# Kernel tuning notes

Hardware: AMD Instinct MI355X
Metric: run time of the kernel (lower is better)

The kernel has to match this reference:

```python
import jax, jax.numpy as jnp
import numpy as np

NEG_INF = -1e30  # log-domain 'zero' (avoid -inf for numerical safety)


def ctc_loss(labels, logits, label_length, logit_length, blank_index=0):
    """Per-example CTC negative log-likelihood.

    labels:       [B, L] int, dense, padded (values != blank within label_length)
    logits:       [T, B, V] float, time-major (TF ctc_loss_v2 default)
    label_length: [B] int
    logit_length: [B] int
    returns:      [B] float, -log p(labels | logits)
    """
    T, B, V = logits.shape
    L = labels.shape[1]
    S = 2 * L + 1  # extended label sequence: blank, l1, blank, l2, ..., blank

    logp = jax.nn.log_softmax(logits, axis=-1)  # [T, B, V]

    # Extended label sequence per batch element: ext[:, 0::2] = blank, ext[:, 1::2] = labels
    ext = jnp.full((B, S), blank_index, dtype=labels.dtype)
    ext = ext.at[:, 1::2].set(labels)  # [B, S]

    # Emission log-probs for each extended position: emit[t, b, s] = logp[t, b, ext[b, s]]
    emit = jnp.take_along_axis(
        logp, jnp.broadcast_to(ext[None].astype(jnp.int32), (T, B, S)), axis=2
    )  # [T, B, S]

    # Skip transition s-2 -> s allowed iff ext[s] != blank and ext[s] != ext[s-2]
    ext_m2 = jnp.concatenate(
        [jnp.full((B, 2), -1, dtype=labels.dtype), ext[:, :-2]], axis=1
    )
    skip_ok = (ext != blank_index) & (ext != ext_m2)  # [B, S]

    def shift(a, k):
        # shift right along S by k, filling with NEG_INF
        return jnp.concatenate(
            [jnp.full((B, k), NEG_INF, dtype=a.dtype), a[:, :-k]], axis=1
        )

    # alpha at t=0: only positions 0 (blank) and 1 (first label) are reachable
    alpha0 = jnp.full((B, S), NEG_INF, dtype=logits.dtype)
    alpha0 = alpha0.at[:, 0].set(emit[0, :, 0]).at[:, 1].set(emit[0, :, 1])

    def step(alpha, xs):
        emit_t, t = xs  # emit_t: [B, S], t: scalar time index
        cand = jnp.stack(
            [alpha, shift(alpha, 1), jnp.where(skip_ok, shift(alpha, 2), NEG_INF)],
            axis=0,
        )  # [3, B, S]
        new = jax.nn.logsumexp(cand, axis=0) + emit_t
        # Freeze alpha for samples whose logit sequence has ended
        new = jnp.where((t < logit_length)[:, None], new, alpha)
        return new, None

    ts = jnp.arange(1, T)
    alpha, _ = jax.lax.scan(step, alpha0, (emit[1:], ts))  # [B, S]

    b = jnp.arange(B)
    end = 2 * label_length  # index of trailing blank for each sample
    ll = jnp.logaddexp(alpha[b, end], alpha[b, jnp.maximum(end - 1, 0)])
    return -ll  # [B]


def setup_inputs() -> dict:
    key = jax.random.key(0)
    k1, k2, k3 = jax.random.split(key, 3)
    T, B, V, L = 1024, 64, 256, 256
    logits = jax.random.normal(k1, (T, B, V), dtype=jnp.float32)
    # labels avoid the blank index (0)
    labels = jax.random.randint(k2, (B, L), 1, V, dtype=jnp.int32)
    label_length = jax.random.randint(k3, (B,), L // 2, L + 1, dtype=jnp.int32)
    logit_length = jnp.full((B,), T, dtype=jnp.int32)
    return {
        "labels": labels,
        "logits": logits,
        "label_length": label_length,
        "logit_length": logit_length,
    }


def reference(labels, logits, label_length, logit_length):
    # CTCLossEndpointCpu: loss = reduce_mean(ctc_loss_v2(...)) with blank_index=0
    per_example = ctc_loss(labels, logits, label_length, logit_length, blank_index=0)
    return jnp.mean(per_example)
```

## Files before the change

### kernel.cpp

```cpp
#include <hip/hip_runtime.h>
#include <math.h>


constexpr int V = 256;
constexpr float LN2_F = 0.6931471805599453f;

typedef unsigned uint2v __attribute__((ext_vector_type(2)));

template <int CTRL>
__device__ __forceinline__ float dpp_mov_f(float x) {
    return __int_as_float(__builtin_amdgcn_update_dpp(
        0, __float_as_int(x), CTRL, 0xF, 0xF, true));
}

__device__ __forceinline__ float wave_shr1_f(float x) {
    return __int_as_float(__builtin_amdgcn_update_dpp(
        0, __float_as_int(x), 0x138, 0xF, 0xF, true));
}

__device__ __forceinline__ float wave_max_f(float m) {
    m = fmaxf(m, dpp_mov_f<0xB1>(m));
    m = fmaxf(m, dpp_mov_f<0x4E>(m));
    m = fmaxf(m, dpp_mov_f<0x124>(m));
    m = fmaxf(m, dpp_mov_f<0x128>(m));
#if __has_builtin(__builtin_amdgcn_permlane16_swap) && __has_builtin(__builtin_amdgcn_permlane32_swap)
    uint2v a = __builtin_amdgcn_permlane16_swap(__float_as_uint(m),
                                                __float_as_uint(m), false, false);
    m = fmaxf(__uint_as_float(a.x), __uint_as_float(a.y));
    uint2v b = __builtin_amdgcn_permlane32_swap(__float_as_uint(m),
                                                __float_as_uint(m), false, false);
    m = fmaxf(__uint_as_float(b.x), __uint_as_float(b.y));
#else
    m = fmaxf(m, __shfl_xor(m, 16, 64));
    m = fmaxf(m, __shfl_xor(m, 32, 64));
#endif
    return m;
}

__device__ __forceinline__ float wave_sum_f(float s) {
    s += dpp_mov_f<0xB1>(s);
    s += dpp_mov_f<0x4E>(s);
    s += dpp_mov_f<0x124>(s);
    s += dpp_mov_f<0x128>(s);
#if __has_builtin(__builtin_amdgcn_permlane16_swap) && __has_builtin(__builtin_amdgcn_permlane32_swap)
    uint2v a = __builtin_amdgcn_permlane16_swap(__float_as_uint(s),
                                                __float_as_uint(s), false, false);
    s = __uint_as_float(a.x) + __uint_as_float(a.y);
    uint2v b = __builtin_amdgcn_permlane32_swap(__float_as_uint(s),
                                                __float_as_uint(s), false, false);
    s = __uint_as_float(b.x) + __uint_as_float(b.y);
#else
    s += __shfl_xor(s, 16, 64);
    s += __shfl_xor(s, 32, 64);
#endif
    return s;
}

#define MACS(EB, E1, E3, E5, E7) do {                                  \
    const float c7m = wave_shr1_f(cur7);                               \
    curT = (curT + cur7) * (EB);                                       \
    cur7 = fmaf(sk7, cur5, cur7 + cur6) * (E7);                        \
    cur6 = (cur6 + cur5) * (EB);                                       \
    cur5 = fmaf(sk5, cur3, cur5 + cur4) * (E5);                        \
    cur4 = (cur4 + cur3) * (EB);                                       \
    cur3 = fmaf(sk3, cur1, cur3 + cur2) * (E3);                        \
    cur2 = (cur2 + cur1) * (EB);                                       \
    cur1 = fmaf(sk1, c7m, cur1 + cur0) * (E1);                         \
    cur0 = (cur0 + c7m) * (EB);                                        \
  } while (0)

#define RENORM do {                                                    \
    curT *= mkT; cur0 *= mk0; cur1 *= mk1; cur2 *= mk2; cur3 *= mk3;   \
    cur4 *= mk4; cur5 *= mk5; cur6 *= mk6; cur7 *= mk7;                \
    float _m = fmaxf(curT, cur0); _m = fmaxf(_m, cur1);                \
    _m = fmaxf(_m, cur2); _m = fmaxf(_m, cur3); _m = fmaxf(_m, cur4);  \
    _m = fmaxf(_m, cur5); _m = fmaxf(_m, cur6); _m = fmaxf(_m, cur7);  \
    _m = wave_max_f(_m);                                               \
    const float _inv = 1.f / fmaxf(_m, 1e-30f);                        \
    log2acc -= log2f(_inv);                                            \
    curT *= _inv; cur0 *= _inv; cur1 *= _inv; cur2 *= _inv;            \
    cur3 *= _inv; cur4 *= _inv; cur5 *= _inv; cur6 *= _inv;            \
    cur7 *= _inv;                                                      \
  } while (0)

#define DECLSET(N) float g##N##a = 0, g##N##b = 0, g##N##c = 0,        \
                         g##N##d = 0, g##N##e = 0
#define PRE(N, S) do {                                                 \
    const float* _er = er + 256 * (S);                                 \
    g##N##a = _er[ix]; g##N##b = _er[iy];                              \
    g##N##c = _er[iz]; g##N##d = _er[iw];                              \
    g##N##e = _er[0];                                                  \
  } while (0)
#define STEPR(N, S) do {                                               \
    MACS(g##N##e, g##N##a, g##N##b, g##N##c, g##N##d);                 \
    PRE(N, S);                                                         \
  } while (0)
#define STEPC(N) MACS(g##N##e, g##N##a, g##N##b, g##N##c, g##N##d)

#define WG_BARRIER asm volatile("s_waitcnt lgkmcnt(0)\n\ts_barrier" ::: "memory")

__global__ __launch_bounds__(1024) void ctc_main(
    const int*   __restrict__ labels,
    const float* __restrict__ logits,
    const int*   __restrict__ label_len,
    const int*   __restrict__ logit_len,
    float*       __restrict__ vres,
    int T, int B, int L)
{
    const int tid = threadIdx.x;
    const int wid = tid >> 6;
    const int l   = tid & 63;
    const int b   = blockIdx.x;

    __shared__ __align__(16) float erow[2][16][256];
    __shared__ float afin[514];
    __shared__ float accbuf[16];

    const int Tb = logit_len[b];
    const int Lb = label_len[b];
    const int NW = Tb / 16;

    const float* lg = logits + (size_t)b * V;
    const size_t rs = (size_t)B * V;

    if (wid == 0) {
        __builtin_amdgcn_s_setprio(1);
        const int Sb = 2 * Lb + 1;

        const int4 lb4 = ((const int4*)(labels + (size_t)b * L))[l];
        const int ix = lb4.x, iy = lb4.y, iz = lb4.z, iw = lb4.w;
        const int prevw = __shfl_up(iw, 1);
        const float sk1 = (l > 0 && ix != prevw) ? 1.f : 0.f;
        const float sk3 = (iy != ix) ? 1.f : 0.f;
        const float sk5 = (iz != iy) ? 1.f : 0.f;
        const float sk7 = (iw != iz) ? 1.f : 0.f;

        const float mk0 = (8 * l + 0 < Sb) ? 1.f : 0.f;
        const float mk1 = (8 * l + 1 < Sb) ? 1.f : 0.f;
        const float mk2 = (8 * l + 2 < Sb) ? 1.f : 0.f;
        const float mk3 = (8 * l + 3 < Sb) ? 1.f : 0.f;
        const float mk4 = (8 * l + 4 < Sb) ? 1.f : 0.f;
        const float mk5 = (8 * l + 5 < Sb) ? 1.f : 0.f;
        const float mk6 = (8 * l + 6 < Sb) ? 1.f : 0.f;
        const float mk7 = (8 * l + 7 < Sb) ? 1.f : 0.f;
        const float mkT = (Sb > 512 && l == 63) ? 1.f : 0.f;

        float cur0 = 0.f, cur1 = 0.f, cur2 = 0.f, cur3 = 0.f;
        float cur4 = 0.f, cur5 = 0.f, cur6 = 0.f, cur7 = 0.f, curT = 0.f;
        if (l == 0) {
            cur0 = __expf(lg[0]);
            cur1 = __expf(lg[ix]) * mk1;
        }
        float log2acc = 0.f;

        DECLSET(0); DECLSET(1); DECLSET(2); DECLSET(3);
        DECLSET(4); DECLSET(5); DECLSET(6); DECLSET(7);

        for (int k = 0; k <= NW; ++k) {
            if (k >= 1) {
                const int w = k - 1;
                const float* er = &erow[w & 1][0][0];
                if (w == 0) {
                    PRE(1, 1); PRE(2, 2); PRE(3, 3); PRE(4, 4);
                    PRE(5, 5); PRE(6, 6); PRE(7, 7); PRE(0, 8);
                    STEPR(1, 9);  STEPR(2, 10); STEPR(3, 11); STEPR(4, 12);
                    STEPR(5, 13); STEPR(6, 14); STEPR(7, 15);
                    STEPC(0);
                    STEPC(1); STEPC(2); STEPC(3); STEPC(4);
                    STEPC(5); STEPC(6); STEPC(7);
                } else {
                    PRE(0, 0); PRE(1, 1); PRE(2, 2); PRE(3, 3);
                    PRE(4, 4); PRE(5, 5); PRE(6, 6); PRE(7, 7);
                    STEPR(0, 8);  STEPR(1, 9);  STEPR(2, 10); STEPR(3, 11);
                    STEPR(4, 12); STEPR(5, 13); STEPR(6, 14); STEPR(7, 15);
                    STEPC(0); STEPC(1); STEPC(2); STEPC(3);
                    STEPC(4); STEPC(5); STEPC(6); STEPC(7);
                }
                RENORM;
            }
            WG_BARRIER;
        }

        for (int t = 16 * NW; t < Tb; ++t) {
            if (t < 1) continue;
            const float* rowp = lg + rs * (size_t)t;
            const float eb = __expf(rowp[0]);
            const float e1 = __expf(rowp[ix]), e3 = __expf(rowp[iy]);
            const float e5 = __expf(rowp[iz]), e7 = __expf(rowp[iw]);
            MACS(eb, e1, e3, e5, e7);
        }

        afin[8 * l + 0] = cur0; afin[8 * l + 1] = cur1;
        afin[8 * l + 2] = cur2; afin[8 * l + 3] = cur3;
        afin[8 * l + 4] = cur4; afin[8 * l + 5] = cur5;
        afin[8 * l + 6] = cur6; afin[8 * l + 7] = cur7;
        if (l == 63) afin[512] = curT;
        const int end = 2 * Lb;
        const int em1 = (end > 0) ? end - 1 : 0;
        float ssum = afin[end] + afin[em1];
        ssum = fmaxf(ssum, 1e-37f);
        const float lnt = logf(ssum) + LN2_F * log2acc;

        WG_BARRIER;

        float c = 0.f;
        #pragma unroll
        for (int q = 0; q < 16; ++q) c += accbuf[q];
        if (l == 0) vres[b] = c - lnt;
    } else {
        const int s0   = wid - 1;
        const bool dual = (wid == 15);
        float accA = 0.f, accB = 0.f;

        float4 pc0{}, pn0{}, pc1{}, pn1{};
        if (NW > 0) {
            pc0 = *(const float4*)(lg + rs * (size_t)s0 + 4 * l);
            pn0 = *(const float4*)(lg + rs * (size_t)(16 + s0) + 4 * l);
            if (dual) {
                pc1 = *(const float4*)(lg + rs * (size_t)15 + 4 * l);
                pn1 = *(const float4*)(lg + rs * (size_t)31 + 4 * l);
            }
        }

        for (int k = 0; k <= NW; ++k) {
            if (k < NW) {
                const int hh = k & 1;
                const float4 x0 = pc0;
                pc0 = pn0;
                if (k + 2 < NW)
                    pn0 = *(const float4*)(lg + rs * (size_t)(16 * (k + 2) + s0) + 4 * l);
                float4 x1{};
                if (dual) {
                    x1 = pc1;
                    pc1 = pn1;
                    if (k + 2 < NW)
                        pn1 = *(const float4*)(lg + rs * (size_t)(16 * (k + 2) + 15) + 4 * l);
                }
                float4 e0;
                e0.x = __expf(x0.x); e0.y = __expf(x0.y);
                e0.z = __expf(x0.z); e0.w = __expf(x0.w);
                *(float4*)&erow[hh][s0][4 * l] = e0;
                if (dual) {
                    float4 e1v;
                    e1v.x = __expf(x1.x); e1v.y = __expf(x1.y);
                    e1v.z = __expf(x1.z); e1v.w = __expf(x1.w);
                    *(float4*)&erow[hh][15][4 * l] = e1v;
                }
                {
                    float m = fmaxf(fmaxf(x0.x, x0.y), fmaxf(x0.z, x0.w));
                    m = wave_max_f(m);
                    float ss = __expf(x0.x - m) + __expf(x0.y - m) +
                               __expf(x0.z - m) + __expf(x0.w - m);
                    ss = wave_sum_f(ss);
                    const int t = 16 * k + s0;
                    if (t < Tb) accA += m + logf(ss);
                }
                if (dual) {
                    float m = fmaxf(fmaxf(x1.x, x1.y), fmaxf(x1.z, x1.w));
                    m = wave_max_f(m);
                    float ss = __expf(x1.x - m) + __expf(x1.y - m) +
                               __expf(x1.z - m) + __expf(x1.w - m);
                    ss = wave_sum_f(ss);
                    const int t = 16 * k + 15;
                    if (t < Tb) accB += m + logf(ss);
                }
            }
            WG_BARRIER;
        }

        for (int t = 16 * NW + s0; t < Tb; t += 16) {
            const float4 x = *(const float4*)(lg + rs * (size_t)t + 4 * l);
            float m = fmaxf(fmaxf(x.x, x.y), fmaxf(x.z, x.w));
            m = wave_max_f(m);
            float ss = __expf(x.x - m) + __expf(x.y - m) +
                       __expf(x.z - m) + __expf(x.w - m);
            ss = wave_sum_f(ss);
            accA += m + logf(ss);
        }
        if (dual) {
            for (int t = 16 * NW + 15; t < Tb; t += 16) {
                const float4 x = *(const float4*)(lg + rs * (size_t)t + 4 * l);
                float m = fmaxf(fmaxf(x.x, x.y), fmaxf(x.z, x.w));
                m = wave_max_f(m);
                float ss = __expf(x.x - m) + __expf(x.y - m) +
                           __expf(x.z - m) + __expf(x.w - m);
                ss = wave_sum_f(ss);
                accB += m + logf(ss);
            }
        }
        if (l == 0) {
            accbuf[s0] = accA;
            if (dual) accbuf[15] = accB;
        }
        WG_BARRIER;
    }
}

__global__ __launch_bounds__(64) void ctc_final(
    const float* __restrict__ vres,
    float* __restrict__ out, int B)
{
    const int b = threadIdx.x;
    float v = (b < B) ? vres[b] : 0.f;
    #pragma unroll
    for (int o = 32; o >= 1; o >>= 1) v += __shfl_xor(v, o, 64);
    if (threadIdx.x == 0) out[0] = v / (float)B;
}

#define FB_PRE(N, S) do {                                              \
    G##N = *(const float4*)(&gbuf[h][S][l][0]);                        \
    A##N = bbuf[h][S];                                                 \
  } while (0)
#define FB_STEPR(N, S) do {                                            \
    MACS(A##N, G##N.x, G##N.y, G##N.z, G##N.w);                        \
    FB_PRE(N, S);                                                      \
  } while (0)
#define FB_STEPC(N) MACS(A##N, G##N.x, G##N.y, G##N.z, G##N.w)

#define FB_PLOAD(dst, WV, J)                                           \
    dst = *(const float4*)(lg + rs * (size_t)(16 * (WV) + p + 7 * (J)) + 4 * l)
#define FB_PROC(XV, i) do {                                            \
    float4 _e;                                                         \
    _e.x = __expf((XV).x); _e.y = __expf((XV).y);                      \
    _e.z = __expf((XV).z); _e.w = __expf((XV).w);                      \
    *(float4*)&prow[p][4 * l] = _e;                                    \
    const float* _pr = prow[p];                                        \
    float _gb = _pr[0];                                                \
    float4 _gv;                                                        \
    _gv.x = _pr[ix]; _gv.y = _pr[iy]; _gv.z = _pr[iz]; _gv.w = _pr[iw];\
    *(float4*)&gbuf[h][i][l][0] = _gv;                                 \
    if (l == 0) bbuf[h][i] = _gb;                                      \
  } while (0)

__global__ __launch_bounds__(512) void fb_ctc_main(
    const int*   __restrict__ labels,
    const float* __restrict__ logits,
    const int*   __restrict__ label_len,
    const int*   __restrict__ logit_len,
    float*       __restrict__ partial,
    float*       __restrict__ lnterm,
    int T, int B, int L)
{
    const int tid = threadIdx.x;
    const int wid = tid >> 6;
    const int l   = tid & 63;

    if ((int)blockIdx.x < B) {
        __shared__ __align__(16) float gbuf[2][16][64][4];
        __shared__ float bbuf[2][16];
        __shared__ __align__(16) float prow[7][256];
        __shared__ float afin[514];

        const int b = blockIdx.x;
        const int Tb = logit_len[b];
        const int Lb = label_len[b];
        const int Sb = 2 * Lb + 1;

        const float* lg = logits + (size_t)b * V;
        const size_t rs = (size_t)B * V;

        const int4 lb4 = ((const int4*)(labels + (size_t)b * L))[l];
        const int ix = lb4.x, iy = lb4.y, iz = lb4.z, iw = lb4.w;
        const int prevw = __shfl_up(iw, 1);
        const float sk1 = (l > 0 && ix != prevw) ? 1.f : 0.f;
        const float sk3 = (iy != ix) ? 1.f : 0.f;
        const float sk5 = (iz != iy) ? 1.f : 0.f;
        const float sk7 = (iw != iz) ? 1.f : 0.f;

        const float mk0 = (8 * l + 0 < Sb) ? 1.f : 0.f;
        const float mk1 = (8 * l + 1 < Sb) ? 1.f : 0.f;
        const float mk2 = (8 * l + 2 < Sb) ? 1.f : 0.f;
        const float mk3 = (8 * l + 3 < Sb) ? 1.f : 0.f;
        const float mk4 = (8 * l + 4 < Sb) ? 1.f : 0.f;
        const float mk5 = (8 * l + 5 < Sb) ? 1.f : 0.f;
        const float mk6 = (8 * l + 6 < Sb) ? 1.f : 0.f;
        const float mk7 = (8 * l + 7 < Sb) ? 1.f : 0.f;
        const float mkT = (Sb > 512 && l == 63) ? 1.f : 0.f;

        float cur0 = 0.f, cur1 = 0.f, cur2 = 0.f, cur3 = 0.f;
        float cur4 = 0.f, cur5 = 0.f, cur6 = 0.f, cur7 = 0.f, curT = 0.f;
        if (l == 0) {
            cur0 = __expf(lg[0]);
            cur1 = __expf(lg[ix]) * mk1;
        }
        float log2acc = 0.f;

        const int NW = Tb / 16;

        float4 G0{}, G1{}, G2{}, G3{}, G4{}, G5{}, G6{}, G7{};
        float  A0 = 0, A1 = 0, A2 = 0, A3 = 0, A4 = 0, A5 = 0, A6 = 0, A7 = 0;

        const int p = (wid > 0) ? wid - 1 : 0;
        const bool three = (p < 2);
        float4 ca{}, cb{}, cc{}, na{}, nb{}, nc{};
        if (wid > 0 && NW > 0) {
            FB_PLOAD(ca, 0, 0);
            FB_PLOAD(cb, 0, 1);
            if (three) FB_PLOAD(cc, 0, 2);
        }
        if (wid == 0) __builtin_amdgcn_s_setprio(1);

        for (int k = 0; k <= NW; ++k) {
            if (wid != 0) {
                if (k < NW) {
                    const int h = k & 1;
                    if (k + 1 < NW) {
                        FB_PLOAD(na, k + 1, 0);
                        FB_PLOAD(nb, k + 1, 1);
                        if (three) FB_PLOAD(nc, k + 1, 2);
                    }
                    FB_PROC(ca, p);
                    FB_PROC(cb, p + 7);
                    if (three) FB_PROC(cc, p + 14);
                    ca = na; cb = nb; cc = nc;
                }
            } else if (k >= 1) {
                const int w = k - 1;
                const int h = w & 1;
                if (w == 0) {
                    FB_PRE(1, 1); FB_PRE(2, 2); FB_PRE(3, 3); FB_PRE(4, 4);
                    FB_PRE(5, 5); FB_PRE(6, 6); FB_PRE(7, 7); FB_PRE(0, 8);
                    FB_STEPR(1, 9);  FB_STEPR(2, 10); FB_STEPR(3, 11);
                    FB_STEPR(4, 12); FB_STEPR(5, 13); FB_STEPR(6, 14);
                    FB_STEPR(7, 15);
                    FB_STEPC(0);
                    FB_STEPC(1); FB_STEPC(2); FB_STEPC(3); FB_STEPC(4);
                    FB_STEPC(5); FB_STEPC(6); FB_STEPC(7);
                } else {
                    FB_PRE(0, 0); FB_PRE(1, 1); FB_PRE(2, 2); FB_PRE(3, 3);
                    FB_PRE(4, 4); FB_PRE(5, 5); FB_PRE(6, 6); FB_PRE(7, 7);
                    FB_STEPR(0, 8);  FB_STEPR(1, 9);  FB_STEPR(2, 10);
                    FB_STEPR(3, 11); FB_STEPR(4, 12); FB_STEPR(5, 13);
                    FB_STEPR(6, 14); FB_STEPR(7, 15);
                    FB_STEPC(0); FB_STEPC(1); FB_STEPC(2); FB_STEPC(3);
                    FB_STEPC(4); FB_STEPC(5); FB_STEPC(6); FB_STEPC(7);
                }
                RENORM;
            }
            WG_BARRIER;
        }

        if (wid == 0) {
            for (int t = 16 * NW; t < Tb; ++t) {
                if (t < 1) continue;
                const float* rowp = lg + rs * (size_t)t;
                const float eb = __expf(rowp[0]);
                const float e1 = __expf(rowp[ix]), e3 = __expf(rowp[iy]);
                const float e5 = __expf(rowp[iz]), e7 = __expf(rowp[iw]);
                MACS(eb, e1, e3, e5, e7);
            }

            afin[8 * l + 0] = cur0; afin[8 * l + 1] = cur1;
            afin[8 * l + 2] = cur2; afin[8 * l + 3] = cur3;
            afin[8 * l + 4] = cur4; afin[8 * l + 5] = cur5;
            afin[8 * l + 6] = cur6; afin[8 * l + 7] = cur7;
            if (l == 63) afin[512] = curT;
            const int end = 2 * Lb;
            const int em1 = (end > 0) ? end - 1 : 0;
            float ssum = afin[end] + afin[em1];
            ssum = fmaxf(ssum, 1e-37f);
            if (l == 0) lnterm[b] = logf(ssum) + LN2_F * log2acc;
        }
    } else {
        const int w  = ((int)blockIdx.x - B) * 8 + wid;
        const int nW = ((int)gridDim.x - B) * 8;
        const int rows = T * B;
        const int bb = w % B;
        const int Tbb = logit_len[bb];
        float acc = 0.f;
        int r = w;
        if (r < rows) {
            int t = w / B;
            const int ts = nW / B;
            float4 nxt = ((const float4*)(logits + (size_t)r * V))[l];
            while (true) {
                const int rn = r + nW;
                const bool more = rn < rows;
                const float4 x = nxt;
                if (more) nxt = ((const float4*)(logits + (size_t)rn * V))[l];
                float m = fmaxf(fmaxf(x.x, x.y), fmaxf(x.z, x.w));
                m = wave_max_f(m);
                float ss = __expf(x.x - m) + __expf(x.y - m) +
                           __expf(x.z - m) + __expf(x.w - m);
                ss = wave_sum_f(ss);
                if (t < Tbb) acc += m + logf(ss);
                if (!more) break;
                r = rn; t += ts;
            }
        }
        if (l == 0) partial[w] = acc;
    }
}

__global__ __launch_bounds__(64) void fb_ctc_final(
    const float* __restrict__ partial,
    const float* __restrict__ lnterm,
    float* __restrict__ out, int B, int nW)
{
    const int b = threadIdx.x;
    float v = 0.f;
    if (b < B) {
        float c = 0.f;
        for (int k = b; k < nW; k += B) c += partial[k];
        v = c - lnterm[b];
    }
    #pragma unroll
    for (int o = 32; o >= 1; o >>= 1) v += __shfl_xor(v, o, 64);
    if (threadIdx.x == 0) out[0] = v / (float)B;
}

extern "C" void kernel_launch(void* const* d_in, const int* in_sizes, int n_in,
                              void* d_out, int out_size, void* d_ws, size_t ws_size,
                              hipStream_t stream) {
    const int*   labels    = (const int*)d_in[0];
    const float* logits    = (const float*)d_in[1];
    const int*   label_len = (const int*)d_in[2];
    const int*   logit_len = (const int*)d_in[3];

    const int B = in_sizes[2];
    const int L = in_sizes[0] / B;
    const int T = in_sizes[1] / (B * V);

    if (T == 1024 && B == 64 && L == 256 && ws_size >= (size_t)B * sizeof(float)) {
        float* vres = (float*)d_ws;
        ctc_main<<<B, 1024, 0, stream>>>(labels, logits, label_len, logit_len,
                                         vres, T, B, L);
        ctc_final<<<1, 64, 0, stream>>>(vres, (float*)d_out, B);
    } else {
        const int nLse = 1024;
        float* partial = (float*)d_ws;
        float* lnterm  = partial + nLse;
        fb_ctc_main<<<B + nLse / 8, 512, 0, stream>>>(labels, logits,
                                                      label_len, logit_len,
                                                      partial, lnterm,
                                                      T, B, L);
        fb_ctc_final<<<1, 64, 0, stream>>>(partial, lnterm, (float*)d_out,
                                           B, nLse);
    }
}
```

Baseline: 174.4 us.

## Pre-gather label emissions in producer waves into packed per-lane LDS buffer

Producer waves now write exp(logits) to a scratch row and immediately gather the four label-indexed entries plus the blank entry per lane. They store these packed as a float4 per lane and a scalar per timestep in a double-buffered layout. The serial recursion wave then reads one aligned float4 and one broadcast scalar per step instead of five scattered LDS reads. This takes gather latency and bank conflicts off the critical path. The cost is extra LDS traffic and work in the producer waves, and a single shared scratch row that depends on wave-local write-then-read ordering.

```diff
diff --git a/kernel.cpp b/kernel.cpp
--- a/kernel.cpp
+++ b/kernel.cpp
@@ -83,19 +83,15 @@
     cur7 *= _inv;                                                      \
   } while (0)
 
-#define DECLSET(N) float g##N##a = 0, g##N##b = 0, g##N##c = 0,        \
-                         g##N##d = 0, g##N##e = 0
 #define PRE(N, S) do {                                                 \
-    const float* _er = er + 256 * (S);                                 \
-    g##N##a = _er[ix]; g##N##b = _er[iy];                              \
-    g##N##c = _er[iz]; g##N##d = _er[iw];                              \
-    g##N##e = _er[0];                                                  \
+    G##N = *(const float4*)(&gbuf[h][S][l][0]);                        \
+    A##N = bbuf[h][S];                                                 \
   } while (0)
 #define STEPR(N, S) do {                                               \
-    MACS(g##N##e, g##N##a, g##N##b, g##N##c, g##N##d);                 \
+    MACS(A##N, G##N.x, G##N.y, G##N.z, G##N.w);                        \
     PRE(N, S);                                                         \
   } while (0)
-#define STEPC(N) MACS(g##N##e, g##N##a, g##N##b, g##N##c, g##N##d)
+#define STEPC(N) MACS(A##N, G##N.x, G##N.y, G##N.z, G##N.w)
 
 #define WG_BARRIER asm volatile("s_waitcnt lgkmcnt(0)\n\ts_barrier" ::: "memory")
 
@@ -112,7 +108,9 @@
     const int l   = tid & 63;
     const int b   = blockIdx.x;
 
-    __shared__ __align__(16) float erow[2][16][256];
+    __shared__ __align__(16) float gbuf[2][16][64][4];
+    __shared__ float bbuf[2][16];
+    __shared__ __align__(16) float prow[16][256];
     __shared__ float afin[514];
     __shared__ float accbuf[16];
 
@@ -123,12 +121,13 @@
     const float* lg = logits + (size_t)b * V;
     const size_t rs = (size_t)B * V;
 
+    const int4 lb4 = ((const int4*)(labels + (size_t)b * L))[l];
+    const int ix = lb4.x, iy = lb4.y, iz = lb4.z, iw = lb4.w;
+
     if (wid == 0) {
         __builtin_amdgcn_s_setprio(1);
         const int Sb = 2 * Lb + 1;
 
-        const int4 lb4 = ((const int4*)(labels + (size_t)b * L))[l];
-        const int ix = lb4.x, iy = lb4.y, iz = lb4.z, iw = lb4.w;
         const int prevw = __shfl_up(iw, 1);
         const float sk1 = (l > 0 && ix != prevw) ? 1.f : 0.f;
         const float sk3 = (iy != ix) ? 1.f : 0.f;
@@ -153,13 +152,13 @@
         }
         float log2acc = 0.f;
 
-        DECLSET(0); DECLSET(1); DECLSET(2); DECLSET(3);
-        DECLSET(4); DECLSET(5); DECLSET(6); DECLSET(7);
+        float4 G0{}, G1{}, G2{}, G3{}, G4{}, G5{}, G6{}, G7{};
+        float  A0 = 0, A1 = 0, A2 = 0, A3 = 0, A4 = 0, A5 = 0, A6 = 0, A7 = 0;
 
         for (int k = 0; k <= NW; ++k) {
             if (k >= 1) {
                 const int w = k - 1;
-                const float* er = &erow[w & 1][0][0];
+                const int h = w & 1;
                 if (w == 0) {
                     PRE(1, 1); PRE(2, 2); PRE(3, 3); PRE(4, 4);
                     PRE(5, 5); PRE(6, 6); PRE(7, 7); PRE(0, 8);
@@ -239,12 +238,21 @@
                 float4 e0;
                 e0.x = __expf(x0.x); e0.y = __expf(x0.y);
                 e0.z = __expf(x0.z); e0.w = __expf(x0.w);
-                *(float4*)&erow[hh][s0][4 * l] = e0;
+                *(float4*)&prow[s0][4 * l] = e0;
                 if (dual) {
                     float4 e1v;
                     e1v.x = __expf(x1.x); e1v.y = __expf(x1.y);
                     e1v.z = __expf(x1.z); e1v.w = __expf(x1.w);
-                    *(float4*)&erow[hh][15][4 * l] = e1v;
+                    *(float4*)&prow[15][4 * l] = e1v;
+                }
+                const float ga = prow[s0][ix], gb2 = prow[s0][iy];
+                const float gc = prow[s0][iz], gd = prow[s0][iw];
+                const float ge = prow[s0][0];
+                float ha = 0, hb = 0, hc = 0, hd = 0, he = 0;
+                if (dual) {
+                    ha = prow[15][ix]; hb = prow[15][iy];
+                    hc = prow[15][iz]; hd = prow[15][iw];
+                    he = prow[15][0];
                 }
                 {
                     float m = fmaxf(fmaxf(x0.x, x0.y), fmaxf(x0.z, x0.w));
@@ -263,6 +271,16 @@
                     ss = wave_sum_f(ss);
                     const int t = 16 * k + 15;
                     if (t < Tb) accB += m + logf(ss);
+                }
+                float4 gv;
+                gv.x = ga; gv.y = gb2; gv.z = gc; gv.w = gd;
+                *(float4*)&gbuf[hh][s0][l][0] = gv;
+                if (l == 0) bbuf[hh][s0] = ge;
+                if (dual) {
+                    float4 hv;
+                    hv.x = ha; hv.y = hb; hv.z = hc; hv.w = hd;
+                    *(float4*)&gbuf[hh][15][l][0] = hv;
+                    if (l == 0) bbuf[hh][15] = he;
                 }
             }
             WG_BARRIER;
```

New measurement: 180.5 us. 3.4% more time.
